# Kernel tuning notes

Hardware: AMD Instinct MI355X
Metric: run time of the kernel (lower is better)

The kernel has to match this reference:

```python
import jax, jax.numpy as jnp
import numpy as np

SIGMA_PRIOR = 0.5   # sigma init kwarg; logvar_prior = log(sigma), sigma_prior = exp(logvar_prior) = sigma
TEMP = 1.0
LN_EPS = 1e-5
DIM, NQ, NK = 256, 512, 512


def setup_inputs() -> dict:
    key = jax.random.key(0)
    ks = jax.random.split(key, 10)
    s = 1.0 / np.sqrt(DIM)
    return {
        "Q": jax.random.normal(ks[0], (NQ, DIM), jnp.float32),
        "K": jax.random.normal(ks[1], (NK, DIM), jnp.float32),
        "V": jax.random.normal(ks[2], (NK, DIM), jnp.float32),
        "eps": jax.random.normal(ks[3], (NQ, NK), jnp.float32),
        # prior MLP: Linear(dim,dim) -> ReLU -> Linear(dim,1)
        "W1p": jax.random.normal(ks[4], (DIM, DIM), jnp.float32) * s,
        "b1p": jnp.zeros((DIM,), jnp.float32),
        "w2p": jax.random.normal(ks[5], (DIM,), jnp.float32) * s,
        "b2p": jnp.zeros((), jnp.float32),
        # posterior MLP: Linear(2*dim, dim) -> ReLU
        "Wpost": jax.random.normal(ks[6], (DIM, 2 * DIM), jnp.float32) * s,
        "bpost": jnp.zeros((DIM,), jnp.float32),
        # mu / logvar heads: Linear(dim, 1)
        "w_mu": jax.random.normal(ks[7], (DIM,), jnp.float32) * s,
        "b_mu": jnp.zeros((), jnp.float32),
        "w_lv": jax.random.normal(ks[8], (DIM,), jnp.float32) * s,
        "b_lv": jnp.zeros((), jnp.float32),
        # output LayerNorm(dim)
        "gamma": jnp.ones((DIM,), jnp.float32),
        "beta": jnp.zeros((DIM,), jnp.float32),
    }


def reference(Q, K, V, eps, W1p, b1p, w2p, b2p, Wpost, bpost,
              w_mu, b_mu, w_lv, b_lv, gamma, beta):
    dim = Q.shape[-1]
    sigma_prior = jnp.float32(SIGMA_PRIOR)

    # --- prior: mlp_prior(K) per key; broadcast over queries (identical math to K_exp) ---
    h = jax.nn.relu(K @ W1p.T + b1p)                       # [Nk, dim]
    mu_prior = h @ w2p + b2p - 0.5 * sigma_prior ** 2      # [Nk]

    # --- posterior: Linear on cat([Q_exp, K_exp]) == Q@Wq^T + K@Wk^T + b ---
    Wq, Wk = Wpost[:, :dim], Wpost[:, dim:]
    latent = jax.nn.relu((Q @ Wq.T)[:, None, :] + (K @ Wk.T + bpost)[None, :, :])  # [Nq, Nk, dim]
    phi = latent @ w_mu + b_mu                             # [Nq, Nk]
    logvar = latent @ w_lv + b_lv                          # [Nq, Nk]
    sig = jnp.exp(0.5 * logvar)
    mu = phi - 0.5 * sig ** 2

    # --- KL(prior || posterior form used by the module) ---
    term0 = jnp.log(sigma_prior / sig)
    term1 = (sig ** 2 + (mu - mu_prior[None, :]) ** 2) / (2.0 * sigma_prior ** 2)
    kl = jnp.mean(term0 + term1 - 0.5)

    # --- reparameterized sample, softmax weights, context ---
    samples = jnp.exp(mu + sig * eps) / TEMP               # [Nq, Nk]
    weights = jax.nn.softmax(samples, axis=-1)
    context = weights @ V                                  # [Nq, dim]

    # --- LayerNorm(dim) ---
    m = jnp.mean(context, axis=-1, keepdims=True)
    v = jnp.var(context, axis=-1, keepdims=True)
    out = (context - m) / jnp.sqrt(v + LN_EPS) * gamma + beta
    return (out, kl)
```

## Files before the change

kernel.cpp:

```cpp
#include <hip/hip_runtime.h>
#include <math.h>

#define DIM 256
#define NQ  512
#define NK  512

#define WS_A   0
#define WS_B   (NQ*DIM)
#define WS_MP  (WS_B + NK*DIM)
#define WS_S   (WS_MP + 512)
#define WS_P   (WS_S + NQ*NK)

__global__ __launch_bounds__(512) void k1_precompute(
    const float* __restrict__ Q, const float* __restrict__ Km,
    const float* __restrict__ W1p, const float* __restrict__ b1p,
    const float* __restrict__ w2p, const float* __restrict__ b2p,
    const float* __restrict__ Wpost, const float* __restrict__ bpost,
    float* __restrict__ A, float* __restrict__ B, float* __restrict__ mu_prior)
{
    __shared__ float X_lds[4][DIM];
    __shared__ float red[2][4][260];
    const int tid = threadIdx.x;
    const int bid = blockIdx.x;

    const int job = bid >> 7;
    const int r0  = (bid & 127) * 4;
    const float* X = (job == 0) ? Q : Km;
    const float* W = (job == 2) ? W1p : Wpost;
    const int wstride = (job == 2) ? DIM : 2 * DIM;
    const int wcol    = (job == 1) ? DIM : 0;

    if (tid < 256) {
        int row = tid >> 6, c4 = tid & 63;
        *(float4*)&X_lds[row][c4 * 4] = *(const float4*)&X[(r0 + row) * DIM + c4 * 4];
    }
    __syncthreads();

    const int c  = tid & 255;
    const int dh = tid >> 8;
    const float* wrow = W + c * wstride + wcol + dh * 128;
    const float* xrow0 = &X_lds[0][dh * 128];

    float acc0 = 0.f, acc1 = 0.f, acc2 = 0.f, acc3 = 0.f;
    #pragma unroll 8
    for (int d0 = 0; d0 < 128; d0 += 4) {
        float4 w4 = *(const float4*)&wrow[d0];
        float4 x0 = *(const float4*)&xrow0[d0];
        float4 x1 = *(const float4*)&xrow0[DIM + d0];
        float4 x2 = *(const float4*)&xrow0[2 * DIM + d0];
        float4 x3 = *(const float4*)&xrow0[3 * DIM + d0];
        acc0 = fmaf(x0.x, w4.x, acc0); acc0 = fmaf(x0.y, w4.y, acc0);
        acc0 = fmaf(x0.z, w4.z, acc0); acc0 = fmaf(x0.w, w4.w, acc0);
        acc1 = fmaf(x1.x, w4.x, acc1); acc1 = fmaf(x1.y, w4.y, acc1);
        acc1 = fmaf(x1.z, w4.z, acc1); acc1 = fmaf(x1.w, w4.w, acc1);
        acc2 = fmaf(x2.x, w4.x, acc2); acc2 = fmaf(x2.y, w4.y, acc2);
        acc2 = fmaf(x2.z, w4.z, acc2); acc2 = fmaf(x2.w, w4.w, acc2);
        acc3 = fmaf(x3.x, w4.x, acc3); acc3 = fmaf(x3.y, w4.y, acc3);
        acc3 = fmaf(x3.z, w4.z, acc3); acc3 = fmaf(x3.w, w4.w, acc3);
    }
    red[dh][0][c] = acc0; red[dh][1][c] = acc1;
    red[dh][2][c] = acc2; red[dh][3][c] = acc3;
    __syncthreads();

    if (job < 2) {
        if (tid < 256) {
            #pragma unroll
            for (int r = 0; r < 4; ++r) {
                float v = red[0][r][c] + red[1][r][c];
                if (job == 0) A[(r0 + r) * DIM + c] = v;
                else          B[(r0 + r) * DIM + c] = v + bpost[c];
            }
        }
    } else {
        if (tid < 256) {
            float b1 = b1p[c], w2 = w2p[c];
            #pragma unroll
            for (int r = 0; r < 4; ++r)
                red[0][r][c] = fmaxf(red[0][r][c] + red[1][r][c] + b1, 0.f) * w2;
        }
        __syncthreads();
        int w = tid >> 6, lane = tid & 63;
        if (w < 4) {
            float v = red[0][w][lane] + red[0][w][lane + 64]
                    + red[0][w][lane + 128] + red[0][w][lane + 192];
            #pragma unroll
            for (int off = 32; off; off >>= 1) v += __shfl_xor(v, off);
            if (lane == 0) mu_prior[r0 + w] = v + b2p[0] - 0.125f;
        }
    }
}

__global__ __launch_bounds__(512) void k2_latent(
    const float* __restrict__ A, const float* __restrict__ B,
    const float* __restrict__ mu_prior, const float* __restrict__ eps,
    const float* __restrict__ w_mu, const float* __restrict__ b_mu,
    const float* __restrict__ w_lv, const float* __restrict__ b_lv,
    float* __restrict__ samples, float* __restrict__ partials)
{
    __shared__ float A_lds[32][260];
    __shared__ float B_lds[32][260];
    __shared__ float wm[DIM], wl[DIM];
    __shared__ float red[2][256][9];
    __shared__ float wred[8];
    const int tid = threadIdx.x;
    const int bq0 = (blockIdx.x >> 4) * 32;
    const int bk0 = (blockIdx.x & 15) * 32;

    #pragma unroll
    for (int i = 0; i < 4; ++i) {
        int f4 = tid + 512 * i;
        int row = f4 >> 6, c4 = f4 & 63;
        *(float4*)&A_lds[row][c4 * 4] = *(const float4*)&A[(bq0 + row) * DIM + c4 * 4];
        *(float4*)&B_lds[row][c4 * 4] = *(const float4*)&B[(bk0 + row) * DIM + c4 * 4];
    }
    if (tid < 256) { wm[tid] = w_mu[tid]; wl[tid] = w_lv[tid]; }
    __syncthreads();

    const int l  = tid & 255;
    const int dh = tid >> 8;
    const int tq = l >> 4, tk = l & 15;
    const int db = dh * 128;

    float p00 = 0, p01 = 0, p10 = 0, p11 = 0;
    float l00 = 0, l01 = 0, l10 = 0, l11 = 0;

    #pragma unroll 4
    for (int dd = 0; dd < 128; dd += 4) {
        int d0 = db + dd;
        float4 a0 = *(const float4*)&A_lds[tq][d0];
        float4 a1 = *(const float4*)&A_lds[tq + 16][d0];
        float4 b0 = *(const float4*)&B_lds[tk][d0];
        float4 b1 = *(const float4*)&B_lds[tk + 16][d0];
        float4 m4 = *(const float4*)&wm[d0];
        float4 v4 = *(const float4*)&wl[d0];
#define STEP(c) { float r_;                                                      \
        r_ = fmaxf(a0.c + b0.c, 0.f); p00 = fmaf(r_, m4.c, p00); l00 = fmaf(r_, v4.c, l00); \
        r_ = fmaxf(a0.c + b1.c, 0.f); p01 = fmaf(r_, m4.c, p01); l01 = fmaf(r_, v4.c, l01); \
        r_ = fmaxf(a1.c + b0.c, 0.f); p10 = fmaf(r_, m4.c, p10); l10 = fmaf(r_, v4.c, l10); \
        r_ = fmaxf(a1.c + b1.c, 0.f); p11 = fmaf(r_, m4.c, p11); l11 = fmaf(r_, v4.c, l11); }
        STEP(x) STEP(y) STEP(z) STEP(w)
#undef STEP
    }

    red[dh][l][0] = p00; red[dh][l][1] = l00;
    red[dh][l][2] = p01; red[dh][l][3] = l01;
    red[dh][l][4] = p10; red[dh][l][5] = l10;
    red[dh][l][6] = p11; red[dh][l][7] = l11;
    __syncthreads();

    float kls = 0.f;
    if (tid < 256) {
        const float bmu = b_mu[0], blv = b_lv[0];
        const int qa = bq0 + tq, qb = qa + 16;
        const int ka = bk0 + tk, kb = ka + 16;
        const float mpa = mu_prior[ka], mpb = mu_prior[kb];
        const float C0 = -0.69314718056f - 0.5f;

#define FINISH(i, q, k, mp) {                                        \
        float pacc = red[0][tid][2*(i)]   + red[1][tid][2*(i)];      \
        float lacc = red[0][tid][2*(i)+1] + red[1][tid][2*(i)+1];    \
        float lv   = lacc + blv;                                     \
        float phi  = pacc + bmu;                                     \
        float sig  = __expf(0.5f * lv);                              \
        float sig2 = sig * sig;                                      \
        float mu   = phi - 0.5f * sig2;                              \
        float dm   = mu - (mp);                                      \
        kls += C0 - 0.5f * lv + 2.f * (sig2 + dm * dm);              \
        samples[(q) * NK + (k)] = __expf(mu + sig * eps[(q) * NK + (k)]); }

        FINISH(0, qa, ka, mpa)
        FINISH(1, qa, kb, mpb)
        FINISH(2, qb, ka, mpa)
        FINISH(3, qb, kb, mpb)
#undef FINISH
    }

    #pragma unroll
    for (int off = 32; off; off >>= 1) kls += __shfl_xor(kls, off);
    if ((tid & 63) == 0) wred[tid >> 6] = kls;
    __syncthreads();
    if (tid == 0) {
        float s = 0.f;
        #pragma unroll
        for (int i = 0; i < 8; ++i) s += wred[i];
        partials[blockIdx.x] = s;
    }
}

__global__ __launch_bounds__(512) void k3_output(
    const float* __restrict__ samples, const float* __restrict__ V,
    const float* __restrict__ gamma, const float* __restrict__ beta,
    const float* __restrict__ partials, float* __restrict__ out)
{
    __shared__ float w_lds[2][NK];
    __shared__ float redbuf[16][DIM];
    __shared__ float sred[8], sred2[8], klr[8], sinv[2];
    const int tid = threadIdx.x;
    const int q0 = blockIdx.x * 2;

    if (blockIdx.x == 0) {
        float v = (tid < 256) ? partials[tid] : 0.f;
        #pragma unroll
        for (int off = 32; off; off >>= 1) v += __shfl_xor(v, off);
        if ((tid & 63) == 0) klr[tid >> 6] = v;
        __syncthreads();
        if (tid == 0) {
            float s = 0.f;
            #pragma unroll
            for (int i = 0; i < 8; ++i) s += klr[i];
            out[NQ * DIM] = s * (1.f / (float)(NQ * NK));
        }
    }

    #pragma unroll
    for (int r = 0; r < 2; ++r) {
        float sv = samples[(q0 + r) * NK + tid];
        float m = sv;
        #pragma unroll
        for (int off = 32; off; off >>= 1) m = fmaxf(m, __shfl_xor(m, off));
        if ((tid & 63) == 0) sred[tid >> 6] = m;
        __syncthreads();
        m = fmaxf(fmaxf(fmaxf(sred[0], sred[1]), fmaxf(sred[2], sred[3])),
                  fmaxf(fmaxf(sred[4], sred[5]), fmaxf(sred[6], sred[7])));
        float e = __expf(sv - m);
        w_lds[r][tid] = e;
        float sum = e;
        #pragma unroll
        for (int off = 32; off; off >>= 1) sum += __shfl_xor(sum, off);
        __syncthreads();
        if ((tid & 63) == 0) sred[tid >> 6] = sum;
        __syncthreads();
        if (tid == 0) {
            float s = 0.f;
            #pragma unroll
            for (int i = 0; i < 8; ++i) s += sred[i];
            sinv[r] = 1.f / s;
        }
        __syncthreads();
    }

    const int g = tid & 63, s = tid >> 6;
    float a00 = 0, a01 = 0, a02 = 0, a03 = 0;
    float a10 = 0, a11 = 0, a12 = 0, a13 = 0;
    const float* vp = V + s * 64 * DIM + 4 * g;
    #pragma unroll 8
    for (int i = 0; i < 64; ++i) {
        float4 v4 = *(const float4*)(vp + i * DIM);
        int k = s * 64 + i;
        float w0 = w_lds[0][k], w1 = w_lds[1][k];
        a00 = fmaf(w0, v4.x, a00); a01 = fmaf(w0, v4.y, a01);
        a02 = fmaf(w0, v4.z, a02); a03 = fmaf(w0, v4.w, a03);
        a10 = fmaf(w1, v4.x, a10); a11 = fmaf(w1, v4.y, a11);
        a12 = fmaf(w1, v4.z, a12); a13 = fmaf(w1, v4.w, a13);
    }
    *(float4*)&redbuf[s * 2 + 0][4 * g] = make_float4(a00, a01, a02, a03);
    *(float4*)&redbuf[s * 2 + 1][4 * g] = make_float4(a10, a11, a12, a13);
    __syncthreads();

    const int r = tid >> 8, col = tid & 255;
    float c = 0.f;
    #pragma unroll
    for (int j = 0; j < 8; ++j) c += redbuf[j * 2 + r][col];
    c *= sinv[r];
    float s1v = c, s2v = c * c;
    #pragma unroll
    for (int off = 32; off; off >>= 1) {
        s1v += __shfl_xor(s1v, off);
        s2v += __shfl_xor(s2v, off);
    }
    if ((tid & 63) == 0) { sred[tid >> 6] = s1v; sred2[tid >> 6] = s2v; }
    __syncthreads();
    float mean = (sred[4 * r] + sred[4 * r + 1] + sred[4 * r + 2] + sred[4 * r + 3]) * (1.f / DIM);
    float msq  = (sred2[4 * r] + sred2[4 * r + 1] + sred2[4 * r + 2] + sred2[4 * r + 3]) * (1.f / DIM);
    float var  = msq - mean * mean;
    out[(q0 + r) * DIM + col] = (c - mean) * rsqrtf(var + 1e-5f) * gamma[col] + beta[col];
}

extern "C" void kernel_launch(void* const* d_in, const int* in_sizes, int n_in,
                              void* d_out, int out_size, void* d_ws, size_t ws_size,
                              hipStream_t stream)
{
    (void)in_sizes; (void)n_in; (void)out_size; (void)ws_size;
    const float* Q     = (const float*)d_in[0];
    const float* K     = (const float*)d_in[1];
    const float* V     = (const float*)d_in[2];
    const float* eps   = (const float*)d_in[3];
    const float* W1p   = (const float*)d_in[4];
    const float* b1p   = (const float*)d_in[5];
    const float* w2p   = (const float*)d_in[6];
    const float* b2p   = (const float*)d_in[7];
    const float* Wpost = (const float*)d_in[8];
    const float* bpost = (const float*)d_in[9];
    const float* w_mu  = (const float*)d_in[10];
    const float* b_mu  = (const float*)d_in[11];
    const float* w_lv  = (const float*)d_in[12];
    const float* b_lv  = (const float*)d_in[13];
    const float* gamma = (const float*)d_in[14];
    const float* beta  = (const float*)d_in[15];
    float* out = (float*)d_out;
    float* wsf = (float*)d_ws;

    float* A        = wsf + WS_A;
    float* B        = wsf + WS_B;
    float* mu_prior = wsf + WS_MP;
    float* samples  = wsf + WS_S;
    float* partials = wsf + WS_P;

    k1_precompute<<<dim3(384), dim3(512), 0, stream>>>(
        Q, K, W1p, b1p, w2p, b2p, Wpost, bpost, A, B, mu_prior);
    k2_latent<<<dim3(256), dim3(512), 0, stream>>>(
        A, B, mu_prior, eps, w_mu, b_mu, w_lv, b_lv, samples, partials);
    k3_output<<<dim3(256), dim3(512), 0, stream>>>(
        samples, V, gamma, beta, partials, out);
}
```

Before: 123.2 us.

## Convert V to fp16 in precompute, merge softmax reductions, spread k2 finish

```diff
diff --git a/kernel.cpp b/kernel.cpp
--- a/kernel.cpp
+++ b/kernel.cpp
@@ -1,4 +1,5 @@
 #include <hip/hip_runtime.h>
+#include <hip/hip_fp16.h>
 #include <math.h>
 
 #define DIM 256
@@ -10,20 +11,34 @@
 #define WS_MP  (WS_B + NK*DIM)
 #define WS_S   (WS_MP + 512)
 #define WS_P   (WS_S + NQ*NK)
+#define WS_VH  (WS_P + 256)
 
 __global__ __launch_bounds__(512) void k1_precompute(
     const float* __restrict__ Q, const float* __restrict__ Km,
+    const float* __restrict__ V,
     const float* __restrict__ W1p, const float* __restrict__ b1p,
     const float* __restrict__ w2p, const float* __restrict__ b2p,
     const float* __restrict__ Wpost, const float* __restrict__ bpost,
-    float* __restrict__ A, float* __restrict__ B, float* __restrict__ mu_prior)
+    float* __restrict__ A, float* __restrict__ B, float* __restrict__ mu_prior,
+    __half2* __restrict__ Vh2)
 {
     __shared__ float X_lds[4][DIM];
     __shared__ float red[2][4][260];
     const int tid = threadIdx.x;
     const int bid = blockIdx.x;
-
     const int job = bid >> 7;
+
+    if (job == 3) {
+        const int pb = (bid - 384) * 4096 + tid;
+        #pragma unroll
+        for (int j = 0; j < 8; ++j) {
+            int p = pb + 512 * j;
+            float2 f = ((const float2*)V)[p];
+            Vh2[p] = __floats2half2_rn(f.x, f.y);
+        }
+        return;
+    }
+
     const int r0  = (bid & 127) * 4;
     const float* X = (job == 0) ? Q : Km;
     const float* W = (job == 2) ? W1p : Wpost;
@@ -149,29 +164,30 @@
     __syncthreads();
 
     float kls = 0.f;
-    if (tid < 256) {
+    {
         const float bmu = b_mu[0], blv = b_lv[0];
-        const int qa = bq0 + tq, qb = qa + 16;
-        const int ka = bk0 + tk, kb = ka + 16;
-        const float mpa = mu_prior[ka], mpb = mu_prior[kb];
+        const int l2 = tid & 255;
+        const int ih = tid >> 8;
+        const int tq2 = l2 >> 4, tk2 = l2 & 15;
+        const int q_  = bq0 + tq2 + 16 * ih;
+        const int ka_ = bk0 + tk2, kb_ = ka_ + 16;
+        const float mpa = mu_prior[ka_], mpb = mu_prior[kb_];
         const float C0 = -0.69314718056f - 0.5f;
 
-#define FINISH(i, q, k, mp) {                                        \
-        float pacc = red[0][tid][2*(i)]   + red[1][tid][2*(i)];      \
-        float lacc = red[0][tid][2*(i)+1] + red[1][tid][2*(i)+1];    \
-        float lv   = lacc + blv;                                     \
-        float phi  = pacc + bmu;                                     \
-        float sig  = __expf(0.5f * lv);                              \
-        float sig2 = sig * sig;                                      \
-        float mu   = phi - 0.5f * sig2;                              \
-        float dm   = mu - (mp);                                      \
-        kls += C0 - 0.5f * lv + 2.f * (sig2 + dm * dm);              \
-        samples[(q) * NK + (k)] = __expf(mu + sig * eps[(q) * NK + (k)]); }
-
-        FINISH(0, qa, ka, mpa)
-        FINISH(1, qa, kb, mpb)
-        FINISH(2, qb, ka, mpa)
-        FINISH(3, qb, kb, mpb)
+#define FINISH(i, k, mp) {                                          \
+        float pacc = red[0][l2][2*(i)]   + red[1][l2][2*(i)];       \
+        float lacc = red[0][l2][2*(i)+1] + red[1][l2][2*(i)+1];     \
+        float lv   = lacc + blv;                                    \
+        float phi  = pacc + bmu;                                    \
+        float sig  = __expf(0.5f * lv);                             \
+        float sig2 = sig * sig;                                     \
+        float mu   = phi - 0.5f * sig2;                             \
+        float dm   = mu - (mp);                                     \
+        kls += C0 - 0.5f * lv + 2.f * (sig2 + dm * dm);             \
+        samples[q_ * NK + (k)] = __expf(mu + sig * eps[q_ * NK + (k)]); }
+
+        FINISH(2 * ih,     ka_, mpa)
+        FINISH(2 * ih + 1, kb_, mpb)
 #undef FINISH
     }
 
@@ -188,21 +204,22 @@
 }
 
 __global__ __launch_bounds__(512) void k3_output(
-    const float* __restrict__ samples, const float* __restrict__ V,
+    const float* __restrict__ samples, const __half2* __restrict__ Vh2,
     const float* __restrict__ gamma, const float* __restrict__ beta,
     const float* __restrict__ partials, float* __restrict__ out)
 {
     __shared__ float w_lds[2][NK];
     __shared__ float redbuf[16][DIM];
-    __shared__ float sred[8], sred2[8], klr[8], sinv[2];
+    __shared__ float sred[8][2], ssum[8][2], klr[8], lnred[8][2];
     const int tid = threadIdx.x;
     const int q0 = blockIdx.x * 2;
+    const int wv = tid >> 6, lane = tid & 63;
 
     if (blockIdx.x == 0) {
         float v = (tid < 256) ? partials[tid] : 0.f;
         #pragma unroll
         for (int off = 32; off; off >>= 1) v += __shfl_xor(v, off);
-        if ((tid & 63) == 0) klr[tid >> 6] = v;
+        if (lane == 0) klr[wv] = v;
         __syncthreads();
         if (tid == 0) {
             float s = 0.f;
@@ -212,46 +229,55 @@
         }
     }
 
-    #pragma unroll
-    for (int r = 0; r < 2; ++r) {
-        float sv = samples[(q0 + r) * NK + tid];
-        float m = sv;
-        #pragma unroll
-        for (int off = 32; off; off >>= 1) m = fmaxf(m, __shfl_xor(m, off));
-        if ((tid & 63) == 0) sred[tid >> 6] = m;
-        __syncthreads();
-        m = fmaxf(fmaxf(fmaxf(sred[0], sred[1]), fmaxf(sred[2], sred[3])),
-                  fmaxf(fmaxf(sred[4], sred[5]), fmaxf(sred[6], sred[7])));
-        float e = __expf(sv - m);
-        w_lds[r][tid] = e;
-        float sum = e;
-        #pragma unroll
-        for (int off = 32; off; off >>= 1) sum += __shfl_xor(sum, off);
-        __syncthreads();
-        if ((tid & 63) == 0) sred[tid >> 6] = sum;
-        __syncthreads();
-        if (tid == 0) {
-            float s = 0.f;
-            #pragma unroll
-            for (int i = 0; i < 8; ++i) s += sred[i];
-            sinv[r] = 1.f / s;
-        }
-        __syncthreads();
-    }
+    float s0 = samples[q0 * NK + tid];
+    float s1 = samples[(q0 + 1) * NK + tid];
+    float m0 = s0, m1 = s1;
+    #pragma unroll
+    for (int off = 32; off; off >>= 1) {
+        m0 = fmaxf(m0, __shfl_xor(m0, off));
+        m1 = fmaxf(m1, __shfl_xor(m1, off));
+    }
+    if (lane == 0) { sred[wv][0] = m0; sred[wv][1] = m1; }
+    __syncthreads();
+    m0 = sred[0][0]; m1 = sred[0][1];
+    #pragma unroll
+    for (int i = 1; i < 8; ++i) {
+        m0 = fmaxf(m0, sred[i][0]);
+        m1 = fmaxf(m1, sred[i][1]);
+    }
+    float e0 = __expf(s0 - m0), e1 = __expf(s1 - m1);
+    w_lds[0][tid] = e0;
+    w_lds[1][tid] = e1;
+    float t0 = e0, t1 = e1;
+    #pragma unroll
+    for (int off = 32; off; off >>= 1) {
+        t0 += __shfl_xor(t0, off);
+        t1 += __shfl_xor(t1, off);
+    }
+    if (lane == 0) { ssum[wv][0] = t0; ssum[wv][1] = t1; }
+    __syncthreads();
+    float sum0 = 0.f, sum1 = 0.f;
+    #pragma unroll
+    for (int i = 0; i < 8; ++i) { sum0 += ssum[i][0]; sum1 += ssum[i][1]; }
+    const float inv0 = 1.f / sum0, inv1 = 1.f / sum1;
 
     const int g = tid & 63, s = tid >> 6;
     float a00 = 0, a01 = 0, a02 = 0, a03 = 0;
     float a10 = 0, a11 = 0, a12 = 0, a13 = 0;
-    const float* vp = V + s * 64 * DIM + 4 * g;
+    const __half2* vp = Vh2 + s * 64 * (DIM / 2) + 2 * g;
     #pragma unroll 8
     for (int i = 0; i < 64; ++i) {
-        float4 v4 = *(const float4*)(vp + i * DIM);
+        float2 raw = *(const float2*)(vp + i * (DIM / 2));
+        __half2 h0 = *(__half2*)&raw.x;
+        __half2 h1 = *(__half2*)&raw.y;
+        float2 f0 = __half22float2(h0);
+        float2 f1 = __half22float2(h1);
         int k = s * 64 + i;
         float w0 = w_lds[0][k], w1 = w_lds[1][k];
-        a00 = fmaf(w0, v4.x, a00); a01 = fmaf(w0, v4.y, a01);
-        a02 = fmaf(w0, v4.z, a02); a03 = fmaf(w0, v4.w, a03);
-        a10 = fmaf(w1, v4.x, a10); a11 = fmaf(w1, v4.y, a11);
-        a12 = fmaf(w1, v4.z, a12); a13 = fmaf(w1, v4.w, a13);
+        a00 = fmaf(w0, f0.x, a00); a01 = fmaf(w0, f0.y, a01);
+        a02 = fmaf(w0, f1.x, a02); a03 = fmaf(w0, f1.y, a03);
+        a10 = fmaf(w1, f0.x, a10); a11 = fmaf(w1, f0.y, a11);
+        a12 = fmaf(w1, f1.x, a12); a13 = fmaf(w1, f1.y, a13);
     }
     *(float4*)&redbuf[s * 2 + 0][4 * g] = make_float4(a00, a01, a02, a03);
     *(float4*)&redbuf[s * 2 + 1][4 * g] = make_float4(a10, a11, a12, a13);
@@ -261,17 +287,17 @@
     float c = 0.f;
     #pragma unroll
     for (int j = 0; j < 8; ++j) c += redbuf[j * 2 + r][col];
-    c *= sinv[r];
+    c *= (r == 0) ? inv0 : inv1;
     float s1v = c, s2v = c * c;
     #pragma unroll
     for (int off = 32; off; off >>= 1) {
         s1v += __shfl_xor(s1v, off);
         s2v += __shfl_xor(s2v, off);
     }
-    if ((tid & 63) == 0) { sred[tid >> 6] = s1v; sred2[tid >> 6] = s2v; }
-    __syncthreads();
-    float mean = (sred[4 * r] + sred[4 * r + 1] + sred[4 * r + 2] + sred[4 * r + 3]) * (1.f / DIM);
-    float msq  = (sred2[4 * r] + sred2[4 * r + 1] + sred2[4 * r + 2] + sred2[4 * r + 3]) * (1.f / DIM);
+    if (lane == 0) { lnred[wv][0] = s1v; lnred[wv][1] = s2v; }
+    __syncthreads();
+    float mean = (lnred[4 * r][0] + lnred[4 * r + 1][0] + lnred[4 * r + 2][0] + lnred[4 * r + 3][0]) * (1.f / DIM);
+    float msq  = (lnred[4 * r][1] + lnred[4 * r + 1][1] + lnred[4 * r + 2][1] + lnred[4 * r + 3][1]) * (1.f / DIM);
     float var  = msq - mean * mean;
     out[(q0 + r) * DIM + col] = (c - mean) * rsqrtf(var + 1e-5f) * gamma[col] + beta[col];
 }
@@ -300,16 +326,17 @@
     float* out = (float*)d_out;
     float* wsf = (float*)d_ws;
 
-    float* A        = wsf + WS_A;
-    float* B        = wsf + WS_B;
-    float* mu_prior = wsf + WS_MP;
-    float* samples  = wsf + WS_S;
-    float* partials = wsf + WS_P;
-
-    k1_precompute<<<dim3(384), dim3(512), 0, stream>>>(
-        Q, K, W1p, b1p, w2p, b2p, Wpost, bpost, A, B, mu_prior);
+    float*   A        = wsf + WS_A;
+    float*   B        = wsf + WS_B;
+    float*   mu_prior = wsf + WS_MP;
+    float*   samples  = wsf + WS_S;
+    float*   partials = wsf + WS_P;
+    __half2* Vh2      = (__half2*)(wsf + WS_VH);
+
+    k1_precompute<<<dim3(400), dim3(512), 0, stream>>>(
+        Q, K, V, W1p, b1p, w2p, b2p, Wpost, bpost, A, B, mu_prior, Vh2);
     k2_latent<<<dim3(256), dim3(512), 0, stream>>>(
         A, B, mu_prior, eps, w_mu, b_mu, w_lv, b_lv, samples, partials);
     k3_output<<<dim3(256), dim3(512), 0, stream>>>(
-        samples, V, gamma, beta, partials, out);
+        samples, Vh2, gamma, beta, partials, out);
 }
```

Measured after the change: 123.0 us. Within noise of the previous version (-0.2%).
